# Kernel tuning notes

Measured on AMD Instinct MI355X. Metric: run time of the kernel, lower is better.

Reference implementation:

```python
import jax, jax.numpy as jnp
import numpy as np

H = 16          # num_attention_heads
SCALE = (1024.0 / 16.0) ** 0.5  # attention_head_size = hidden/num_hidden_layers
EPS = 1e-12
NEG = -jnp.inf


def layer_norm(x, g, b):
    mu = jnp.mean(x, axis=-1, keepdims=True)
    var = jnp.mean((x - mu) ** 2, axis=-1, keepdims=True)
    return (x - mu) * jax.lax.rsqrt(var + EPS) * g + b


def setup_inputs() -> dict:
    key = jax.random.key(0)
    ks = jax.random.split(key, 8)
    B, S, D, F = 4, 2048, 1024, 4096
    s = 0.02
    return {
        "hidden_state": jax.random.normal(ks[0], (B, S, D), jnp.float32),
        "attention_mask": jnp.ones((B, S), jnp.int32),
        "Wq": jax.random.normal(ks[1], (D, D), jnp.float32) * s,
        "Wk": jax.random.normal(ks[2], (D, D), jnp.float32) * s,
        "Wv": jax.random.normal(ks[3], (D, D), jnp.float32) * s,
        "Wo": jax.random.normal(ks[4], (D, D), jnp.float32) * s,
        "ln1_g": jnp.ones((D,), jnp.float32),
        "ln1_b": jnp.zeros((D,), jnp.float32),
        "W1": jax.random.normal(ks[5], (D, F), jnp.float32) * s,
        "b1": jnp.zeros((F,), jnp.float32),
        "W2": jax.random.normal(ks[6], (F, D), jnp.float32) * s,
        "b2": jnp.zeros((D,), jnp.float32),
        "ln2_g": jnp.ones((D,), jnp.float32),
        "ln2_b": jnp.zeros((D,), jnp.float32),
    }


def reference(hidden_state, attention_mask, Wq, Wk, Wv, Wo, ln1_g, ln1_b,
              W1, b1, W2, b2, ln2_g, ln2_b):
    B, S, D = hidden_state.shape
    # --- square attention mask (is_not_pad == 1) + causal ---
    amb = attention_mask == 1                              # [B,S] bool
    pair = amb[:, :, None] & amb[:, None, :]               # [B,S,S]
    self_mask = jnp.where(pair, 0.0, NEG)[:, None, :, :]   # [B,1,S,S]
    causal = jnp.where(jnp.triu(jnp.ones((S, S), bool), 1), NEG, 0.0)
    self_mask = self_mask + causal                         # [B,1,S,S]

    # --- self attention (pre-norm) ---
    residual = hidden_state
    x = layer_norm(hidden_state, ln1_g, ln1_b)
    q = (x @ Wq).reshape(B, S, H, D // H)
    k = (x @ Wk).reshape(B, S, H, D // H)
    v = (x @ Wv).reshape(B, S, H, D // H)
    scores = jnp.einsum('bqhd,bkhd->bhqk', q, k) / SCALE + self_mask
    probs = jax.nn.softmax(scores, axis=-1)                # dropout p=0
    ctx = jnp.einsum('bhqk,bkhd->bqhd', probs, v).reshape(B, S, D)
    x = ctx @ Wo + residual

    # --- feed forward (pre-norm, SiLU) ---
    residual = x
    y = layer_norm(x, ln2_g, ln2_b)
    y = jax.nn.silu(y @ W1 + b1) @ W2 + b2
    return y + residual
```

## Files before the change

kernel.cpp:

```cpp
#include <hip/hip_runtime.h>
#include <math.h>

typedef __attribute__((ext_vector_type(8))) short short8;
typedef __attribute__((ext_vector_type(4))) float floatx4;

__device__ __forceinline__ float b2f(ushort u) {
    union { uint i; float f; } c; c.i = ((uint)u) << 16; return c.f;
}
__device__ __forceinline__ ushort f2b(float f) {
    union { float f; uint i; } c; c.f = f;
    return (ushort)((c.i + 0x7fffu + ((c.i >> 16) & 1u)) >> 16);
}

__device__ __forceinline__ void async_cp16(const ushort* g, ushort* l) {
    __builtin_amdgcn_global_load_lds(
        (const __attribute__((address_space(1))) void*)g,
        (__attribute__((address_space(3))) void*)l, 16, 0, 0);
}

__device__ __forceinline__ float dpp_max16(float x) {
    int y;
    y = __builtin_amdgcn_update_dpp(__float_as_int(x), __float_as_int(x), 0xB1, 0xF, 0xF, false);
    x = fmaxf(x, __int_as_float(y));
    y = __builtin_amdgcn_update_dpp(__float_as_int(x), __float_as_int(x), 0x4E, 0xF, 0xF, false);
    x = fmaxf(x, __int_as_float(y));
    y = __builtin_amdgcn_update_dpp(__float_as_int(x), __float_as_int(x), 0x141, 0xF, 0xF, false);
    x = fmaxf(x, __int_as_float(y));
    y = __builtin_amdgcn_update_dpp(__float_as_int(x), __float_as_int(x), 0x140, 0xF, 0xF, false);
    x = fmaxf(x, __int_as_float(y));
    return x;
}

__global__ __launch_bounds__(256) void cvt_t_kernel(
    const float* __restrict__ S, ushort* __restrict__ D, int K, int N)
{
    __shared__ float ls[32][33];
    const int k0 = blockIdx.y * 32, n0 = blockIdx.x * 32;
    const int t = threadIdx.x;
    const int kr = t >> 3, nc = (t & 7) * 4;
    float4 f = *(const float4*)(S + (size_t)(k0 + kr) * N + n0 + nc);
    ls[kr][nc] = f.x; ls[kr][nc + 1] = f.y; ls[kr][nc + 2] = f.z; ls[kr][nc + 3] = f.w;
    __syncthreads();
    const int nr = t >> 3, kc = (t & 7) * 4;
    ushort4 o;
    o.x = f2b(ls[kc][nr]); o.y = f2b(ls[kc + 1][nr]);
    o.z = f2b(ls[kc + 2][nr]); o.w = f2b(ls[kc + 3][nr]);
    *(ushort4*)(D + (size_t)(n0 + nr) * K + k0 + kc) = o;
}

__global__ __launch_bounds__(256) void ln_kernel(
    const float* __restrict__ X, const float* __restrict__ G,
    const float* __restrict__ Bb, ushort* __restrict__ Y)
{
    const int row = blockIdx.x;
    const int t = threadIdx.x;
    const float* xr = X + (size_t)row * 1024;
    float4 p = ((const float4*)xr)[t];
    float s = p.x + p.y + p.z + p.w;
    float s2 = p.x * p.x + p.y * p.y + p.z * p.z + p.w * p.w;
    #pragma unroll
    for (int off = 32; off > 0; off >>= 1) {
        s += __shfl_down(s, off);
        s2 += __shfl_down(s2, off);
    }
    __shared__ float rs1[4], rs2[4];
    if ((t & 63) == 0) { rs1[t >> 6] = s; rs2[t >> 6] = s2; }
    __syncthreads();
    float S1 = rs1[0] + rs1[1] + rs1[2] + rs1[3];
    float S2 = rs2[0] + rs2[1] + rs2[2] + rs2[3];
    float mu = S1 * (1.0f / 1024.0f);
    float var = S2 * (1.0f / 1024.0f) - mu * mu;
    float rstd = rsqrtf(var + 1e-12f);
    float4 gp = ((const float4*)G)[t];
    float4 bp = ((const float4*)Bb)[t];
    ushort4 o;
    o.x = f2b((p.x - mu) * rstd * gp.x + bp.x);
    o.y = f2b((p.y - mu) * rstd * gp.y + bp.y);
    o.z = f2b((p.z - mu) * rstd * gp.z + bp.z);
    o.w = f2b((p.w - mu) * rstd * gp.w + bp.w);
    ((ushort4*)(Y + (size_t)row * 1024))[t] = o;
}

template<int BN, bool BIAS, bool SILU, bool RESID, bool OUTF32>
__global__ __launch_bounds__(256) void gemm_bt_kernel(
    const ushort* __restrict__ A, const ushort* __restrict__ Bt,
    const float* __restrict__ bias, const float* __restrict__ resid,
    void* __restrict__ Cm, int M, int N, int K)
{
    constexpr int NF = BN / 32;
    constexpr int BI = BN / 64;
    __shared__ __align__(16) ushort lsA[128 * 32];
    __shared__ __align__(16) ushort lsB[BN * 32];

    const int t = threadIdx.x;
    const int m0 = blockIdx.y * 128;
    const int n0 = blockIdx.x * BN;
    const int w = t >> 6;
    const int lane = t & 63;
    const int wm = (w >> 1) * 64;
    const int wn = (w & 1) * (BN / 2);
    const int quad = lane >> 4;
    const int l16 = lane & 15;
    const int ko = quad * 8;

    const int lrow = lane >> 2;
    const int scol = (lane & 3) * 8;
    const int srA = w * 32 + lrow;
    const int srB = (BI == 2) ? (w * 32 + lrow) : (w * 16 + lrow);
    const ushort* gA = A + (size_t)(m0 + srA) * K + scol;
    const ushort* gB = Bt + (size_t)(n0 + srB) * K + scol;
    ushort* lA0 = &lsA[(w * 32) * 32];
    ushort* lA1 = &lsA[(w * 32 + 16) * 32];
    ushort* lB0 = (BI == 2) ? &lsB[(w * 32) * 32] : &lsB[(w * 16) * 32];
    ushort* lB1 = (BI == 2) ? &lsB[(w * 32 + 16) * 32] : nullptr;

    floatx4 acc[4][NF];
    #pragma unroll
    for (int i = 0; i < 4; ++i)
        #pragma unroll
        for (int j = 0; j < NF; ++j)
            acc[i][j] = (floatx4){0.f, 0.f, 0.f, 0.f};

    for (int k0 = 0; k0 < K; k0 += 32) {
        __syncthreads();
        async_cp16(gA + k0, lA0);
        async_cp16(gA + (size_t)16 * K + k0, lA1);
        async_cp16(gB + k0, lB0);
        if constexpr (BI == 2) async_cp16(gB + (size_t)16 * K + k0, lB1);
        __syncthreads();

        short8 af[4], bf[NF];
        #pragma unroll
        for (int i = 0; i < 4; ++i)
            af[i] = *(const short8*)&lsA[(wm + i * 16 + l16) * 32 + ko];
        #pragma unroll
        for (int j = 0; j < NF; ++j)
            bf[j] = *(const short8*)&lsB[(wn + j * 16 + l16) * 32 + ko];
        #pragma unroll
        for (int i = 0; i < 4; ++i)
            #pragma unroll
            for (int j = 0; j < NF; ++j)
                acc[i][j] = __builtin_amdgcn_mfma_f32_16x16x32_bf16(
                    af[i], bf[j], acc[i][j], 0, 0, 0);
    }

    #pragma unroll
    for (int tn = 0; tn < NF; ++tn) {
        const int n = n0 + wn + tn * 16 + l16;
        const float bv = BIAS ? bias[n] : 0.0f;
        #pragma unroll
        for (int tm = 0; tm < 4; ++tm) {
            const int mbase = m0 + wm + tm * 16 + quad * 4;
            #pragma unroll
            for (int rr = 0; rr < 4; ++rr) {
                float v = acc[tm][tn][rr] + bv;
                if (SILU) v = v / (1.0f + __expf(-v));
                const size_t off = (size_t)(mbase + rr) * N + n;
                if (RESID) v += resid[off];
                if constexpr (OUTF32) ((float*)Cm)[off] = v;
                else                  ((ushort*)Cm)[off] = f2b(v);
            }
        }
    }
}

__global__ __launch_bounds__(256, 4) void attn_kernel(
    const ushort* __restrict__ Qm, const ushort* __restrict__ Km,
    const ushort* __restrict__ Vm, const int* __restrict__ amask,
    ushort* __restrict__ Om, int rs)
{
    __shared__ __align__(16) ushort lsQP[64][72];
    __shared__ __align__(16) ushort lsK[64][72];
    __shared__ __align__(16) ushort lsVt[64][72];
    __shared__ int lsMk[64];

    const int bh = blockIdx.y;
    const int b = bh >> 4, h = bh & 15;
    const int t = threadIdx.x;
    const int w = t >> 6, lane = t & 63;
    const int quad = lane >> 4, l16 = lane & 15;

    const size_t base = ((size_t)b * 2048) * rs + (size_t)h * 64;
    const size_t obase = ((size_t)b * 2048) * 1024 + (size_t)h * 64;

    const int krow = t >> 3, kc8 = (t & 7) << 3;
    const int vp = t & 31, vc8 = (t >> 5) << 3;
    const float scale2 = 0.125f * 1.44269504f;

    short8 ones8;
    #pragma unroll
    for (int i = 0; i < 8; ++i) ones8[i] = (short)0x3F80;

    #pragma unroll 1
    for (int half = 0; half < 2; ++half) {
        const int qt = half ? blockIdx.x : (31 - blockIdx.x);
        const int q0 = qt * 64;

        __syncthreads();
        #pragma unroll
        for (int it = 0; it < 2; ++it) {
            int idx = it * 256 + t;
            int row = idx >> 3, c8 = (idx & 7) << 3;
            *(int4*)&lsQP[row][c8] =
                *(const int4*)(Qm + base + (size_t)(q0 + row) * rs + c8);
        }
        __syncthreads();

        short8 aq0 = *(const short8*)&lsQP[w * 16 + l16][quad * 8];
        short8 aq1 = *(const short8*)&lsQP[w * 16 + l16][32 + quad * 8];

        floatx4 Oacc[4];
        #pragma unroll
        for (int d = 0; d < 4; ++d) Oacc[d] = (floatx4){0.f, 0.f, 0.f, 0.f};
        floatx4 Lacc = (floatx4){0.f, 0.f, 0.f, 0.f};
        float m_i[4] = {-INFINITY, -INFINITY, -INFINITY, -INFINITY};

        int4 kr0 = *(const int4*)(Km + base + (size_t)krow * rs + kc8);
        int4 kr1 = *(const int4*)(Km + base + (size_t)(32 + krow) * rs + kc8);
        int4 vr0 = *(const int4*)(Vm + base + (size_t)(2 * vp) * rs + vc8);
        int4 vr1 = *(const int4*)(Vm + base + (size_t)(2 * vp + 1) * rs + vc8);
        int mr = amask[b * 2048 + (t & 63)];

        for (int kt = 0; kt <= qt; ++kt) {
            __syncthreads();
            *(int4*)&lsK[krow][kc8] = kr0;
            *(int4*)&lsK[32 + krow][kc8] = kr1;
            {
                const ushort* p0 = (const ushort*)&vr0;
                const ushort* p1 = (const ushort*)&vr1;
                #pragma unroll
                for (int i = 0; i < 8; ++i) {
                    uint pk = (uint)p0[i] | ((uint)p1[i] << 16);
                    *(uint*)&lsVt[vc8 + i][2 * vp] = pk;
                }
            }
            if (t < 64) lsMk[t] = mr;
            __syncthreads();

            if (kt < qt) {
                const int kn = (kt + 1) * 64;
                kr0 = *(const int4*)(Km + base + (size_t)(kn + krow) * rs + kc8);
                kr1 = *(const int4*)(Km + base + (size_t)(kn + 32 + krow) * rs + kc8);
                vr0 = *(const int4*)(Vm + base + (size_t)(kn + 2 * vp) * rs + vc8);
                vr1 = *(const int4*)(Vm + base + (size_t)(kn + 2 * vp + 1) * rs + vc8);
                mr = amask[b * 2048 + kn + (t & 63)];
            }

            floatx4 sa[4];
            #pragma unroll
            for (int j = 0; j < 4; ++j) {
                short8 bk0 = *(const short8*)&lsK[j * 16 + l16][quad * 8];
                short8 bk1 = *(const short8*)&lsK[j * 16 + l16][32 + quad * 8];
                floatx4 z = (floatx4){0.f, 0.f, 0.f, 0.f};
                z = __builtin_amdgcn_mfma_f32_16x16x32_bf16(aq0, bk0, z, 0, 0, 0);
                sa[j] = __builtin_amdgcn_mfma_f32_16x16x32_bf16(aq1, bk1, z, 0, 0, 0);
            }

            float kb[4];
            #pragma unroll
            for (int j = 0; j < 4; ++j)
                kb[j] = (lsMk[j * 16 + l16] == 1) ? 0.f : -INFINITY;
            const bool diag = (kt == qt);

            float sv[4][4];
            float mx[4];
            #pragma unroll
            for (int rr = 0; rr < 4; ++rr) {
                const int qrow = w * 16 + quad * 4 + rr;
                float mxv = -INFINITY;
                #pragma unroll
                for (int j = 0; j < 4; ++j) {
                    float v = sa[j][rr] * scale2 + kb[j];
                    if (diag) v = (j * 16 + l16 <= qrow) ? v : -INFINITY;
                    sv[rr][j] = v;
                    mxv = fmaxf(mxv, v);
                }
                mx[rr] = dpp_max16(mxv);
            }
            int grow = (mx[0] > m_i[0] + 8.0f) | (mx[1] > m_i[1] + 8.0f) |
                       (mx[2] > m_i[2] + 8.0f) | (mx[3] > m_i[3] + 8.0f);
            if (__any(grow)) {
                #pragma unroll
                for (int rr = 0; rr < 4; ++rr) {
                    const float m_new = fmaxf(m_i[rr], mx[rr]);
                    const float al = exp2f(m_i[rr] - m_new);
                    m_i[rr] = m_new;
                    #pragma unroll
                    for (int d = 0; d < 4; ++d) Oacc[d][rr] *= al;
                    Lacc[rr] *= al;
                }
            }
            #pragma unroll
            for (int rr = 0; rr < 4; ++rr) {
                #pragma unroll
                for (int j = 0; j < 4; ++j) {
                    const float p = exp2f(sv[rr][j] - m_i[rr]);
                    lsQP[w * 16 + quad * 4 + rr][j * 16 + l16] =
                        (ushort)(__float_as_uint(p) >> 16);
                }
            }

            short8 ap0 = *(const short8*)&lsQP[w * 16 + l16][quad * 8];
            short8 ap1 = *(const short8*)&lsQP[w * 16 + l16][32 + quad * 8];
            #pragma unroll
            for (int d = 0; d < 4; ++d) {
                short8 bv0 = *(const short8*)&lsVt[d * 16 + l16][quad * 8];
                short8 bv1 = *(const short8*)&lsVt[d * 16 + l16][32 + quad * 8];
                Oacc[d] = __builtin_amdgcn_mfma_f32_16x16x32_bf16(ap0, bv0, Oacc[d], 0, 0, 0);
                Oacc[d] = __builtin_amdgcn_mfma_f32_16x16x32_bf16(ap1, bv1, Oacc[d], 0, 0, 0);
            }
            Lacc = __builtin_amdgcn_mfma_f32_16x16x32_bf16(ap0, ones8, Lacc, 0, 0, 0);
            Lacc = __builtin_amdgcn_mfma_f32_16x16x32_bf16(ap1, ones8, Lacc, 0, 0, 0);
        }

        #pragma unroll
        for (int rr = 0; rr < 4; ++rr) {
            const float inv = 1.0f / Lacc[rr];
            const int row = q0 + w * 16 + quad * 4 + rr;
            ushort* op = Om + obase + (size_t)row * 1024;
            #pragma unroll
            for (int d = 0; d < 4; ++d)
                op[d * 16 + l16] = f2b(Oacc[d][rr] * inv);
        }
    }
}

extern "C" void kernel_launch(void* const* d_in, const int* in_sizes, int n_in,
                              void* d_out, int out_size, void* d_ws, size_t ws_size,
                              hipStream_t stream) {
    const float* hidden = (const float*)d_in[0];
    const int*   amask  = (const int*)d_in[1];
    const float* Wq  = (const float*)d_in[2];
    const float* Wk  = (const float*)d_in[3];
    const float* Wv  = (const float*)d_in[4];
    const float* Wo  = (const float*)d_in[5];
    const float* l1g = (const float*)d_in[6];
    const float* l1b = (const float*)d_in[7];
    const float* W1  = (const float*)d_in[8];
    const float* b1  = (const float*)d_in[9];
    const float* W2  = (const float*)d_in[10];
    const float* b2  = (const float*)d_in[11];
    const float* l2g = (const float*)d_in[12];
    const float* l2b = (const float*)d_in[13];

    const int M = 8192;
    const size_t MB = 1048576;
    char* ws = (char*)d_ws;
    ushort* xa    = (ushort*)(ws);
    ushort* qkvb  = (ushort*)(ws + 16 * MB);
    ushort* Wqkvt = (ushort*)(ws + 64 * MB);
    ushort* Wot   = (ushort*)(ws + 70 * MB);
    ushort* W1t   = (ushort*)(ws);
    ushort* W2t   = (ushort*)(ws + 8 * MB);
    ushort* yb    = (ushort*)(ws + 16 * MB);
    ushort* hbc   = (ushort*)(ws + 32 * MB);
    float*  x2    = (float*)d_out;

    cvt_t_kernel<<<dim3(32, 32), 256, 0, stream>>>(Wq, Wqkvt, 1024, 1024);
    cvt_t_kernel<<<dim3(32, 32), 256, 0, stream>>>(Wk, Wqkvt + (size_t)1024 * 1024, 1024, 1024);
    cvt_t_kernel<<<dim3(32, 32), 256, 0, stream>>>(Wv, Wqkvt + (size_t)2048 * 1024, 1024, 1024);
    cvt_t_kernel<<<dim3(32, 32), 256, 0, stream>>>(Wo, Wot, 1024, 1024);

    ln_kernel<<<M, 256, 0, stream>>>(hidden, l1g, l1b, xa);
    gemm_bt_kernel<128, false, false, false, false><<<dim3(24, 64), 256, 0, stream>>>(
        xa, Wqkvt, nullptr, nullptr, qkvb, M, 3072, 1024);
    attn_kernel<<<dim3(16, 64), 256, 0, stream>>>(
        qkvb, qkvb + 1024, qkvb + 2048, amask, xa, 3072);
    gemm_bt_kernel<64, false, false, true, true><<<dim3(16, 64), 256, 0, stream>>>(
        xa, Wot, nullptr, hidden, x2, M, 1024, 1024);

    cvt_t_kernel<<<dim3(128, 32), 256, 0, stream>>>(W1, W1t, 1024, 4096);
    cvt_t_kernel<<<dim3(32, 128), 256, 0, stream>>>(W2, W2t, 4096, 1024);

    ln_kernel<<<M, 256, 0, stream>>>(x2, l2g, l2b, yb);
    for (int mc = 0; mc < 2; ++mc) {
        const size_t off = (size_t)mc * 4096 * 1024;
        gemm_bt_kernel<128, true, true, false, false><<<dim3(32, 32), 256, 0, stream>>>(
            yb + off, W1t, b1, nullptr, hbc, 4096, 4096, 1024);
        gemm_bt_kernel<64, true, false, true, true><<<dim3(16, 32), 256, 0, stream>>>(
            hbc, W2t, b2, x2 + off, (void*)(x2 + off), 4096, 1024, 4096);
    }
}
```

Baseline: 655.0 us.

## Swizzle GEMM LDS tiles with BK=64, remap blocks, use transposed LDS reads in attention

The GEMM now stages K-tiles of 64 using an XOR-swizzled LDS layout, which removes bank conflicts and halves the number of barriers per K. Workgroup IDs are remapped across 8 chunks, likely to group blocks per XCD for L2 locality. The attention kernel now writes P as packed bf16 with v_cvt_pk_bf16_f32 and reads it back with ds_read_b64_tr_b16 transposed loads. It also defers the DPP row-max reduction until a rescale is actually needed. The LDS footprint doubles and the code now relies on inline asm with manual waitcnt.

```diff
diff --git a/kernel.cpp b/kernel.cpp
--- a/kernel.cpp
+++ b/kernel.cpp
@@ -3,6 +3,7 @@
 
 typedef __attribute__((ext_vector_type(8))) short short8;
 typedef __attribute__((ext_vector_type(4))) float floatx4;
+typedef __attribute__((ext_vector_type(2))) unsigned int uintx2;
 
 __device__ __forceinline__ float b2f(ushort u) {
     union { uint i; float f; } c; c.i = ((uint)u) << 16; return c.f;
@@ -16,6 +17,10 @@
     __builtin_amdgcn_global_load_lds(
         (const __attribute__((address_space(1))) void*)g,
         (__attribute__((address_space(3))) void*)l, 16, 0, 0);
+}
+
+__device__ __forceinline__ uint lds_u32(const void* p) {
+    return (uint)(uintptr_t)(const __attribute__((address_space(3))) void*)p;
 }
 
 __device__ __forceinline__ float dpp_max16(float x) {
@@ -89,30 +94,27 @@
 {
     constexpr int NF = BN / 32;
     constexpr int BI = BN / 64;
-    __shared__ __align__(16) ushort lsA[128 * 32];
-    __shared__ __align__(16) ushort lsB[BN * 32];
+    __shared__ __align__(16) ushort lsA[128 * 64];
+    __shared__ __align__(16) ushort lsB[BN * 64];
 
     const int t = threadIdx.x;
-    const int m0 = blockIdx.y * 128;
-    const int n0 = blockIdx.x * BN;
+    const int L = blockIdx.x + gridDim.x * blockIdx.y;
+    const int cpx = (gridDim.x * gridDim.y) >> 3;
+    const int wg = (L & 7) * cpx + (L >> 3);
+    const int m0 = (wg / gridDim.x) * 128;
+    const int n0 = (wg % gridDim.x) * BN;
     const int w = t >> 6;
     const int lane = t & 63;
     const int wm = (w >> 1) * 64;
     const int wn = (w & 1) * (BN / 2);
     const int quad = lane >> 4;
     const int l16 = lane & 15;
-    const int ko = quad * 8;
-
-    const int lrow = lane >> 2;
-    const int scol = (lane & 3) * 8;
-    const int srA = w * 32 + lrow;
-    const int srB = (BI == 2) ? (w * 32 + lrow) : (w * 16 + lrow);
-    const ushort* gA = A + (size_t)(m0 + srA) * K + scol;
-    const ushort* gB = Bt + (size_t)(n0 + srB) * K + scol;
-    ushort* lA0 = &lsA[(w * 32) * 32];
-    ushort* lA1 = &lsA[(w * 32 + 16) * 32];
-    ushort* lB0 = (BI == 2) ? &lsB[(w * 32) * 32] : &lsB[(w * 16) * 32];
-    ushort* lB1 = (BI == 2) ? &lsB[(w * 32 + 16) * 32] : nullptr;
+
+    const int lrow = lane >> 3;
+    const int scol = ((lane & 7) ^ lrow) * 8;
+    const ushort* gA = A + (size_t)(m0 + w * 32 + lrow) * K + scol;
+    const ushort* gB = Bt + (size_t)(n0 + ((BI == 2) ? w * 32 : w * 16) + lrow) * K + scol;
+    const int sw = l16 & 7;
 
     floatx4 acc[4][NF];
     #pragma unroll
@@ -121,27 +123,39 @@
         for (int j = 0; j < NF; ++j)
             acc[i][j] = (floatx4){0.f, 0.f, 0.f, 0.f};
 
-    for (int k0 = 0; k0 < K; k0 += 32) {
+    for (int k0 = 0; k0 < K; k0 += 64) {
         __syncthreads();
-        async_cp16(gA + k0, lA0);
-        async_cp16(gA + (size_t)16 * K + k0, lA1);
-        async_cp16(gB + k0, lB0);
-        if constexpr (BI == 2) async_cp16(gB + (size_t)16 * K + k0, lB1);
+        #pragma unroll
+        for (int i = 0; i < 4; ++i)
+            async_cp16(gA + k0 + (size_t)(8 * i) * K, &lsA[(w * 32 + 8 * i) * 64]);
+        if constexpr (BI == 2) {
+            #pragma unroll
+            for (int i = 0; i < 4; ++i)
+                async_cp16(gB + k0 + (size_t)(8 * i) * K, &lsB[(w * 32 + 8 * i) * 64]);
+        } else {
+            #pragma unroll
+            for (int i = 0; i < 2; ++i)
+                async_cp16(gB + k0 + (size_t)(8 * i) * K, &lsB[(w * 16 + 8 * i) * 64]);
+        }
         __syncthreads();
 
-        short8 af[4], bf[NF];
-        #pragma unroll
-        for (int i = 0; i < 4; ++i)
-            af[i] = *(const short8*)&lsA[(wm + i * 16 + l16) * 32 + ko];
-        #pragma unroll
-        for (int j = 0; j < NF; ++j)
-            bf[j] = *(const short8*)&lsB[(wn + j * 16 + l16) * 32 + ko];
-        #pragma unroll
-        for (int i = 0; i < 4; ++i)
+        #pragma unroll
+        for (int h = 0; h < 2; ++h) {
+            const int co = (((h << 2) | quad) ^ sw) * 8;
+            short8 af[4], bf[NF];
+            #pragma unroll
+            for (int i = 0; i < 4; ++i)
+                af[i] = *(const short8*)&lsA[(wm + i * 16 + l16) * 64 + co];
             #pragma unroll
             for (int j = 0; j < NF; ++j)
-                acc[i][j] = __builtin_amdgcn_mfma_f32_16x16x32_bf16(
-                    af[i], bf[j], acc[i][j], 0, 0, 0);
+                bf[j] = *(const short8*)&lsB[(wn + j * 16 + l16) * 64 + co];
+            #pragma unroll
+            for (int i = 0; i < 4; ++i)
+                #pragma unroll
+                for (int j = 0; j < NF; ++j)
+                    acc[i][j] = __builtin_amdgcn_mfma_f32_16x16x32_bf16(
+                        af[i], bf[j], acc[i][j], 0, 0, 0);
+        }
     }
 
     #pragma unroll
@@ -174,7 +188,9 @@
     __shared__ __align__(16) ushort lsVt[64][72];
     __shared__ int lsMk[64];
 
-    const int bh = blockIdx.y;
+    const int L = blockIdx.x + (int)(gridDim.x * blockIdx.y);
+    const int bh = L & 63;
+    const int pr = L >> 6;
     const int b = bh >> 4, h = bh & 15;
     const int t = threadIdx.x;
     const int w = t >> 6, lane = t & 63;
@@ -187,13 +203,18 @@
     const int vp = t & 31, vc8 = (t >> 5) << 3;
     const float scale2 = 0.125f * 1.44269504f;
 
+    ushort* strip = &lsQP[w * 16][0];
+    const uint strip_a = lds_u32(strip);
+    char* wp_base = (char*)strip + l16 * 32 + quad * 8;
+    const uint rp = strip_a + quad * 256 + l16 * 8;
+
     short8 ones8;
     #pragma unroll
     for (int i = 0; i < 8; ++i) ones8[i] = (short)0x3F80;
 
     #pragma unroll 1
     for (int half = 0; half < 2; ++half) {
-        const int qt = half ? blockIdx.x : (31 - blockIdx.x);
+        const int qt = half ? pr : (31 - pr);
         const int q0 = qt * 64;
 
         __syncthreads();
@@ -263,7 +284,7 @@
             const bool diag = (kt == qt);
 
             float sv[4][4];
-            float mx[4];
+            float mxl[4];
             #pragma unroll
             for (int rr = 0; rr < 4; ++rr) {
                 const int qrow = w * 16 + quad * 4 + rr;
@@ -275,14 +296,15 @@
                     sv[rr][j] = v;
                     mxv = fmaxf(mxv, v);
                 }
-                mx[rr] = dpp_max16(mxv);
-            }
-            int grow = (mx[0] > m_i[0] + 8.0f) | (mx[1] > m_i[1] + 8.0f) |
-                       (mx[2] > m_i[2] + 8.0f) | (mx[3] > m_i[3] + 8.0f);
+                mxl[rr] = mxv;
+            }
+            int grow = (mxl[0] > m_i[0] + 8.0f) | (mxl[1] > m_i[1] + 8.0f) |
+                       (mxl[2] > m_i[2] + 8.0f) | (mxl[3] > m_i[3] + 8.0f);
             if (__any(grow)) {
                 #pragma unroll
                 for (int rr = 0; rr < 4; ++rr) {
-                    const float m_new = fmaxf(m_i[rr], mx[rr]);
+                    const float mx = dpp_max16(mxl[rr]);
+                    const float m_new = fmaxf(m_i[rr], mx);
                     const float al = exp2f(m_i[rr] - m_new);
                     m_i[rr] = m_new;
                     #pragma unroll
@@ -290,18 +312,33 @@
                     Lacc[rr] *= al;
                 }
             }
-            #pragma unroll
-            for (int rr = 0; rr < 4; ++rr) {
-                #pragma unroll
-                for (int j = 0; j < 4; ++j) {
-                    const float p = exp2f(sv[rr][j] - m_i[rr]);
-                    lsQP[w * 16 + quad * 4 + rr][j * 16 + l16] =
-                        (ushort)(__float_as_uint(p) >> 16);
-                }
-            }
-
-            short8 ap0 = *(const short8*)&lsQP[w * 16 + l16][quad * 8];
-            short8 ap1 = *(const short8*)&lsQP[w * 16 + l16][32 + quad * 8];
+
+            #pragma unroll
+            for (int j = 0; j < 4; ++j) {
+                float p0 = exp2f(sv[0][j] - m_i[0]);
+                float p1 = exp2f(sv[1][j] - m_i[1]);
+                float p2 = exp2f(sv[2][j] - m_i[2]);
+                float p3 = exp2f(sv[3][j] - m_i[3]);
+                uint w0, w1;
+                asm("v_cvt_pk_bf16_f32 %0, %1, %2" : "=v"(w0) : "v"(p0), "v"(p1));
+                asm("v_cvt_pk_bf16_f32 %0, %1, %2" : "=v"(w1) : "v"(p2), "v"(p3));
+                *(uint2*)(wp_base + j * 512) = make_uint2(w0, w1);
+            }
+
+            asm volatile("s_waitcnt lgkmcnt(0)" ::: "memory");
+            uintx2 t0, t1, t2, t3;
+            asm volatile("ds_read_b64_tr_b16 %0, %1 offset:0"    : "=v"(t0) : "v"(rp));
+            asm volatile("ds_read_b64_tr_b16 %0, %1 offset:128"  : "=v"(t1) : "v"(rp));
+            asm volatile("ds_read_b64_tr_b16 %0, %1 offset:1024" : "=v"(t2) : "v"(rp));
+            asm volatile("ds_read_b64_tr_b16 %0, %1 offset:1152" : "=v"(t3) : "v"(rp));
+            asm volatile("s_waitcnt lgkmcnt(0)" ::: "memory");
+            __builtin_amdgcn_sched_barrier(0);
+            union { short8 s; uint u[4]; } ua0, ua1;
+            ua0.u[0] = t0.x; ua0.u[1] = t0.y; ua0.u[2] = t1.x; ua0.u[3] = t1.y;
+            ua1.u[0] = t2.x; ua1.u[1] = t2.y; ua1.u[2] = t3.x; ua1.u[3] = t3.y;
+            const short8 ap0 = ua0.s;
+            const short8 ap1 = ua1.s;
+
             #pragma unroll
             for (int d = 0; d < 4; ++d) {
                 short8 bv0 = *(const short8*)&lsVt[d * 16 + l16][quad * 8];
```

After: 587.7 us. 1.11x faster.
